# Performance work log

Hardware: AMD Instinct MI355X
Metric: run time of the kernel (lower is better)

Reference implementation:

```python
import jax, jax.numpy as jnp
import numpy as np

# Model hyperparameters (match init_kwargs)
D, N, M_DIM, L, BATCH = 10, 500, 5, 6, 1024
W_STD, B_STD, A_STD = 0.1, 0.0, 1.0


def softplus10(x):
    return jax.nn.softplus(10.0 * x) / 10.0


def setup_inputs() -> dict:
    key = jax.random.key(0)
    ks = jax.random.split(key, 7)
    w_scale = W_STD / np.sqrt(M_DIM).astype(np.float32)
    return {
        "X": jax.random.normal(ks[0], (BATCH, D), dtype=jnp.float32),
        "w_first": W_STD * jax.random.normal(ks[1], (D, N, 1, M_DIM), dtype=jnp.float32),
        "w_mid": w_scale * jax.random.normal(ks[2], (L - 2, D, N, M_DIM, M_DIM), dtype=jnp.float32),
        "w_last": w_scale * jax.random.normal(ks[3], (D, N, M_DIM, 1), dtype=jnp.float32),
        "bs": B_STD * jax.random.normal(ks[4], (L - 1, D, N, M_DIM), dtype=jnp.float32),
        "b_last": B_STD * jax.random.normal(ks[5], (D, N, 1), dtype=jnp.float32),
        "a_all": A_STD * jax.random.normal(ks[6], (L - 1, D, N, M_DIM), dtype=jnp.float32),
    }


def reference(X, w_first, w_mid, w_last, bs, b_last, a_all):
    # X: [M, d] -> phis: [M, d, n, 1]
    Mb = X.shape[0]
    phis = jnp.broadcast_to(X[:, :, None, None], (Mb, D, N, 1))
    phidots = jnp.ones_like(phis)  # [M, d, n, 1]

    ws = [w_first] + [w_mid[i] for i in range(L - 2)]
    for l in range(L - 1):
        W = softplus10(ws[l])                                    # [d,n,k,m]
        pre = jnp.einsum('mjik,jikl->mjil', phis, W) + bs[l]     # [M,d,n,m]
        ta = jnp.tanh(a_all[l])                                  # [d,n,m]
        tanhdot = 1.0 - jnp.tanh(pre) ** 2                       # tanh'(pre)
        phidots = jnp.einsum('mjik,jikl->mjil', phidots, W) * (1.0 + ta * tanhdot)
        phis = pre + jnp.tanh(pre) * ta

    Wl = softplus10(w_last)                                      # [d,n,m,1]
    pre = jnp.einsum('mjik,jikl->mjil', phis, Wl) + b_last       # [M,d,n,1]
    s = jax.nn.sigmoid(pre)
    phidots = jnp.einsum('mjik,jikl->mjil', phidots, Wl) * (s * (1.0 - s))

    fm = jax.lax.stop_gradient(-jnp.log(phidots + 1e-10))        # [M,d,n,1]
    fm = jnp.min(jnp.mean(fm, axis=1, keepdims=True), axis=2, keepdims=True)
    return jnp.squeeze(phidots, -1), fm.reshape(-1)              # ([M,d,n], [M])
```

## Files before the change

### kernel.cpp

```cpp
#include <hip/hip_runtime.h>
#include <math.h>

#define D_ 10
#define N_ 500
#define REC 164

typedef float f32x2 __attribute__((ext_vector_type(2)));

__device__ __forceinline__ float fexp2(float x){ float r; asm("v_exp_f32 %0, %1" : "=v"(r) : "v"(x)); return r; }
__device__ __forceinline__ float flog2(float x){ float r; asm("v_log_f32 %0, %1" : "=v"(r) : "v"(x)); return r; }
__device__ __forceinline__ float frcp (float x){ float r; asm("v_rcp_f32 %0, %1" : "=v"(r) : "v"(x)); return r; }

#define LOG2E 1.4426950408889634f
#define LN2   0.6931471805599453f

__device__ __forceinline__ float fast_tanh(float x){
  float e = fexp2(x * (2.0f*LOG2E));
  return 1.0f - 2.0f*frcp(e + 1.0f);
}
__device__ __forceinline__ float softplus10(float x){
  float e = fexp2(x * (10.0f*LOG2E));
  return (0.1f*LN2) * flog2(1.0f + e);
}

__device__ __forceinline__ f32x2 pk_fma_blo(f32x2 a, f32x2 w, f32x2 c){
  f32x2 d; asm("v_pk_fma_f32 %0, %1, %2, %3 op_sel:[0,0,0] op_sel_hi:[1,0,1]"
               : "=v"(d) : "v"(a), "s"(w), "v"(c)); return d; }
__device__ __forceinline__ f32x2 pk_fma_bhi(f32x2 a, f32x2 w, f32x2 c){
  f32x2 d; asm("v_pk_fma_f32 %0, %1, %2, %3 op_sel:[0,1,0] op_sel_hi:[1,1,1]"
               : "=v"(d) : "v"(a), "s"(w), "v"(c)); return d; }
__device__ __forceinline__ f32x2 pk_mul_blo(f32x2 a, f32x2 w){
  f32x2 d; asm("v_pk_mul_f32 %0, %1, %2 op_sel:[0,0] op_sel_hi:[1,0]"
               : "=v"(d) : "v"(a), "s"(w)); return d; }
__device__ __forceinline__ f32x2 pk_mul_bhi(f32x2 a, f32x2 w){
  f32x2 d; asm("v_pk_mul_f32 %0, %1, %2 op_sel:[0,1] op_sel_hi:[1,1]"
               : "=v"(d) : "v"(a), "s"(w)); return d; }
__device__ __forceinline__ f32x2 pk_mul(f32x2 a, f32x2 b){
  f32x2 d; asm("v_pk_mul_f32 %0, %1, %2" : "=v"(d) : "v"(a), "v"(b)); return d; }
__device__ __forceinline__ f32x2 pk_add(f32x2 a, f32x2 b){
  f32x2 d; asm("v_pk_add_f32 %0, %1, %2" : "=v"(d) : "v"(a), "v"(b)); return d; }
__device__ __forceinline__ f32x2 pk_nfma(f32x2 a, f32x2 b, f32x2 c){
  f32x2 d; asm("v_pk_fma_f32 %0, %1, %2, %3 neg_lo:[1,0,0] neg_hi:[1,0,0]"
               : "=v"(d) : "v"(a), "v"(b), "v"(c)); return d; }

#define LD2(off)        (*(const f32x2*)(r + ((off) & ~1)))
#define FMA_B(a, off, c) (((off)&1) ? pk_fma_bhi((a), LD2(off), (c)) : pk_fma_blo((a), LD2(off), (c)))
#define MUL_B(a, off)    (((off)&1) ? pk_mul_bhi((a), LD2(off))      : pk_mul_blo((a), LD2(off)))

__global__ __launch_bounds__(256) void tennet_prep(
    const float* __restrict__ w_first, const float* __restrict__ w_mid,
    const float* __restrict__ w_last, const float* __restrict__ bs,
    const float* __restrict__ b_last, const float* __restrict__ a_all,
    float* __restrict__ rec)
{
  int rid = blockIdx.x*4 + (threadIdx.x >> 6);
  int lane = threadIdx.x & 63;
  int d = rid / N_;
  int n = rid - d*N_;
  float* dst = rec + rid*REC;
  for (int i = lane; i < 161; i += 64) {
    float v;
    if (i < 5)        v = softplus10(w_first[(d*N_+n)*5 + i]);
    else if (i < 10)  v = bs[(d*N_+n)*5 + (i-5)];
    else if (i < 15)  v = fast_tanh(a_all[(d*N_+n)*5 + (i-10)]);
    else if (i < 155) {
      int q = i - 15; int l = q/35; int r2 = q - l*35;
      if (r2 < 25) {
        int j = r2/5, k = r2 - (r2/5)*5;
        v = softplus10(w_mid[((l*D_+d)*N_+n)*25 + k*5 + j]);
      } else if (r2 < 30) {
        v = bs[(((l+1)*D_+d)*N_+n)*5 + (r2-25)];
      } else {
        v = fast_tanh(a_all[(((l+1)*D_+d)*N_+n)*5 + (r2-30)]);
      }
    }
    else if (i < 160) v = softplus10(w_last[(d*N_+n)*5 + (i-155)]);
    else              v = b_last[d*N_+n];
    dst[i] = v;
  }
}

__global__ __launch_bounds__(1024) void tennet_main(
    const float* __restrict__ X, const float* __restrict__ rec,
    float* __restrict__ out0)
{
  __shared__ float tr[128*17];
  int bid = blockIdx.x;
  int mb  = bid & 7;
  int nch = (bid >> 3) & 31;
  int d   = bid >> 8;
  int n0 = nch*16;
  int t = threadIdx.x;
  int wv = __builtin_amdgcn_readfirstlane(t >> 6);
  int lane = t & 63;
  int n = n0 + wv;
  int nr = (n < N_) ? n : (N_-1);
  const float* r = rec + (d*N_ + nr)*REC;
  int m0 = mb*128 + lane;

  f32x2 x;
  x.x = X[m0*D_ + d];
  x.y = X[(m0+64)*D_ + d];

  const f32x2 ONE = {1.0f, 1.0f};
  const f32x2 TWO = {2.0f, 2.0f};
  const f32x2 K2  = {2.0f*LOG2E, 2.0f*LOG2E};
  const f32x2 NL2E = {-LOG2E, -LOG2E};

  f32x2 phis[5], phid[5];
  #pragma unroll
  for (int j = 0; j < 5; ++j) {
    f32x2 pre = FMA_B(x, j, MUL_B(ONE, 5+j));
    f32x2 tt = pk_mul(pre, K2);
    f32x2 e; e.x = fexp2(tt.x); e.y = fexp2(tt.y);
    f32x2 p1 = pk_add(e, ONE);
    f32x2 rc; rc.x = frcp(p1.x); rc.y = frcp(p1.y);
    f32x2 th = pk_nfma(TWO, rc, ONE);
    f32x2 td = pk_nfma(th, th, ONE);
    f32x2 u  = FMA_B(td, 10+j, ONE);
    phid[j] = MUL_B(u, j);
    phis[j] = FMA_B(th, 10+j, pre);
  }
  #pragma unroll
  for (int l = 0; l < 4; ++l) {
    const int base = 15 + l*35;
    f32x2 nphis[5], nphid[5];
    #pragma unroll
    for (int j = 0; j < 5; ++j) {
      f32x2 pre = FMA_B(phis[0], base + j*5, MUL_B(ONE, base + 25 + j));
      f32x2 pd  = MUL_B(phid[0], base + j*5);
      #pragma unroll
      for (int k = 1; k < 5; ++k) {
        pre = FMA_B(phis[k], base + j*5 + k, pre);
        pd  = FMA_B(phid[k], base + j*5 + k, pd);
      }
      f32x2 tt = pk_mul(pre, K2);
      f32x2 e; e.x = fexp2(tt.x); e.y = fexp2(tt.y);
      f32x2 p1 = pk_add(e, ONE);
      f32x2 rc; rc.x = frcp(p1.x); rc.y = frcp(p1.y);
      f32x2 th = pk_nfma(TWO, rc, ONE);
      f32x2 td = pk_nfma(th, th, ONE);
      f32x2 u  = FMA_B(td, base + 30 + j, ONE);
      nphid[j] = pk_mul(pd, u);
      nphis[j] = FMA_B(th, base + 30 + j, pre);
    }
    #pragma unroll
    for (int j = 0; j < 5; ++j){ phis[j]=nphis[j]; phid[j]=nphid[j]; }
  }
  f32x2 pre = FMA_B(phis[0], 155, MUL_B(ONE, 160));
  f32x2 pd  = MUL_B(phid[0], 155);
  #pragma unroll
  for (int k = 1; k < 5; ++k) {
    pre = FMA_B(phis[k], 155 + k, pre);
    pd  = FMA_B(phid[k], 155 + k, pd);
  }
  f32x2 tt = pk_mul(pre, NL2E);
  f32x2 e; e.x = fexp2(tt.x); e.y = fexp2(tt.y);
  f32x2 p1 = pk_add(e, ONE);
  f32x2 sg; sg.x = frcp(p1.x); sg.y = frcp(p1.y);
  f32x2 om = pk_nfma(sg, ONE, ONE);
  f32x2 res = pk_mul(pk_mul(pd, sg), om);

  tr[lane*17 + wv] = res.x;
  tr[(lane+64)*17 + wv] = res.y;
  __syncthreads();
  int tn = t & 15;
  #pragma unroll
  for (int rr = (t >> 4); rr < 128; rr += 64) {
    if (n0 + tn < N_)
      out0[((mb*128 + rr)*D_ + d)*N_ + n0 + tn] = tr[rr*17 + tn];
  }
}

__global__ __launch_bounds__(512) void tennet_fm(
    const float* __restrict__ out0, float* __restrict__ fm)
{
  int m = blockIdx.x;
  int t = threadIdx.x;
  float val = INFINITY;
  if (t < N_) {
    float acc = 0.0f;
    #pragma unroll
    for (int d = 0; d < D_; ++d) {
      float v = out0[(m*D_ + d)*N_ + t];
      acc += flog2(v + 1e-10f);
    }
    val = -acc * (LN2 / (float)D_);
  }
  #pragma unroll
  for (int off = 32; off; off >>= 1) {
    float o = __shfl_down(val, off, 64);
    val = fminf(val, o);
  }
  __shared__ float red[8];
  int wid = t >> 6;
  if ((t & 63) == 0) red[wid] = val;
  __syncthreads();
  if (t == 0) {
    float v = red[0];
    #pragma unroll
    for (int ww = 1; ww < 8; ++ww) v = fminf(v, red[ww]);
    fm[m] = v;
  }
}

extern "C" void kernel_launch(void* const* d_in, const int* in_sizes, int n_in,
                              void* d_out, int out_size, void* d_ws, size_t ws_size,
                              hipStream_t stream) {
  const float* X       = (const float*)d_in[0];
  const float* w_first = (const float*)d_in[1];
  const float* w_mid   = (const float*)d_in[2];
  const float* w_last  = (const float*)d_in[3];
  const float* bs      = (const float*)d_in[4];
  const float* b_last  = (const float*)d_in[5];
  const float* a_all   = (const float*)d_in[6];
  float* out0 = (float*)d_out;
  float* fm   = out0 + 1024*D_*N_;
  float* rec  = (float*)d_ws;

  tennet_prep<<<(D_*N_)/4, 256, 0, stream>>>(w_first, w_mid, w_last, bs, b_last, a_all, rec);
  tennet_main<<<10*32*8, 1024, 0, stream>>>(X, rec, out0);
  tennet_fm<<<1024, 512, 0, stream>>>(out0, fm);
}
```

Baseline: 66.47 us.

## Share one reciprocal across paired lanes and shrink main kernel blocks to 8 waves

The tanh and sigmoid activations now compute a single reciprocal of the product of the two packed denominators and recover each reciprocal with a multiply, halving the transcendental v_rcp count. The main kernel moves from 16 waves per block over 16 n-values to 8 waves over 8 n-values, with a matching grid and transpose buffer. This cuts padding waste (500 n-values now fill 504 slots instead of 512) and gives the scheduler finer blocks. The shared reciprocal risks overflow or underflow when both exp terms are large.

```diff
diff --git a/kernel.cpp b/kernel.cpp
--- a/kernel.cpp
+++ b/kernel.cpp
@@ -46,6 +46,19 @@
 #define LD2(off)        (*(const f32x2*)(r + ((off) & ~1)))
 #define FMA_B(a, off, c) (((off)&1) ? pk_fma_bhi((a), LD2(off), (c)) : pk_fma_blo((a), LD2(off), (c)))
 #define MUL_B(a, off)    (((off)&1) ? pk_mul_bhi((a), LD2(off))      : pk_mul_blo((a), LD2(off)))
+
+__device__ __forceinline__ void act_tanh(f32x2 pre, f32x2 ONE, f32x2 TWO, f32x2 K2,
+                                         f32x2* th, f32x2* td){
+  f32x2 tt = pk_mul(pre, K2);
+  f32x2 e; e.x = fexp2(tt.x); e.y = fexp2(tt.y);
+  f32x2 p1 = pk_add(e, ONE);
+  float pr = p1.x * p1.y;
+  float rr = frcp(pr);
+  f32x2 rc; rc.x = p1.y * rr; rc.y = p1.x * rr;
+  f32x2 t = pk_nfma(TWO, rc, ONE);
+  *th = t;
+  *td = pk_nfma(t, t, ONE);
+}
 
 __global__ __launch_bounds__(256) void tennet_prep(
     const float* __restrict__ w_first, const float* __restrict__ w_mid,
@@ -80,16 +93,17 @@
   }
 }
 
-__global__ __launch_bounds__(1024) void tennet_main(
+__global__ __launch_bounds__(512) void tennet_main(
     const float* __restrict__ X, const float* __restrict__ rec,
     float* __restrict__ out0)
 {
-  __shared__ float tr[128*17];
+  __shared__ float tr[128*9];
   int bid = blockIdx.x;
   int mb  = bid & 7;
-  int nch = (bid >> 3) & 31;
-  int d   = bid >> 8;
-  int n0 = nch*16;
+  int q   = bid >> 3;
+  int d   = q / 63;
+  int nch = q - d*63;
+  int n0 = nch*8;
   int t = threadIdx.x;
   int wv = __builtin_amdgcn_readfirstlane(t >> 6);
   int lane = t & 63;
@@ -111,14 +125,10 @@
   #pragma unroll
   for (int j = 0; j < 5; ++j) {
     f32x2 pre = FMA_B(x, j, MUL_B(ONE, 5+j));
-    f32x2 tt = pk_mul(pre, K2);
-    f32x2 e; e.x = fexp2(tt.x); e.y = fexp2(tt.y);
-    f32x2 p1 = pk_add(e, ONE);
-    f32x2 rc; rc.x = frcp(p1.x); rc.y = frcp(p1.y);
-    f32x2 th = pk_nfma(TWO, rc, ONE);
-    f32x2 td = pk_nfma(th, th, ONE);
-    f32x2 u  = FMA_B(td, 10+j, ONE);
-    phid[j] = MUL_B(u, j);
+    f32x2 th, td;
+    act_tanh(pre, ONE, TWO, K2, &th, &td);
+    f32x2 uf = FMA_B(td, 10+j, ONE);
+    phid[j] = MUL_B(uf, j);
     phis[j] = FMA_B(th, 10+j, pre);
   }
   #pragma unroll
@@ -134,14 +144,10 @@
         pre = FMA_B(phis[k], base + j*5 + k, pre);
         pd  = FMA_B(phid[k], base + j*5 + k, pd);
       }
-      f32x2 tt = pk_mul(pre, K2);
-      f32x2 e; e.x = fexp2(tt.x); e.y = fexp2(tt.y);
-      f32x2 p1 = pk_add(e, ONE);
-      f32x2 rc; rc.x = frcp(p1.x); rc.y = frcp(p1.y);
-      f32x2 th = pk_nfma(TWO, rc, ONE);
-      f32x2 td = pk_nfma(th, th, ONE);
-      f32x2 u  = FMA_B(td, base + 30 + j, ONE);
-      nphid[j] = pk_mul(pd, u);
+      f32x2 th, td;
+      act_tanh(pre, ONE, TWO, K2, &th, &td);
+      f32x2 uf = FMA_B(td, base + 30 + j, ONE);
+      nphid[j] = pk_mul(pd, uf);
       nphis[j] = FMA_B(th, base + 30 + j, pre);
     }
     #pragma unroll
@@ -157,18 +163,21 @@
   f32x2 tt = pk_mul(pre, NL2E);
   f32x2 e; e.x = fexp2(tt.x); e.y = fexp2(tt.y);
   f32x2 p1 = pk_add(e, ONE);
-  f32x2 sg; sg.x = frcp(p1.x); sg.y = frcp(p1.y);
+  float prd = p1.x * p1.y;
+  float rrc = frcp(prd);
+  f32x2 sg; sg.x = p1.y * rrc; sg.y = p1.x * rrc;
   f32x2 om = pk_nfma(sg, ONE, ONE);
   f32x2 res = pk_mul(pk_mul(pd, sg), om);
 
-  tr[lane*17 + wv] = res.x;
-  tr[(lane+64)*17 + wv] = res.y;
+  tr[lane*9 + wv]      = res.x;
+  tr[(lane+64)*9 + wv] = res.y;
   __syncthreads();
-  int tn = t & 15;
-  #pragma unroll
-  for (int rr = (t >> 4); rr < 128; rr += 64) {
+  int tn = t & 7;
+  #pragma unroll
+  for (int p = 0; p < 2; ++p) {
+    int rr2 = (t >> 3) + p*64;
     if (n0 + tn < N_)
-      out0[((mb*128 + rr)*D_ + d)*N_ + n0 + tn] = tr[rr*17 + tn];
+      out0[((mb*128 + rr2)*D_ + d)*N_ + n0 + tn] = tr[rr2*9 + tn];
   }
 }
 
@@ -219,6 +228,6 @@
   float* rec  = (float*)d_ws;
 
   tennet_prep<<<(D_*N_)/4, 256, 0, stream>>>(w_first, w_mid, w_last, bs, b_last, a_all, rec);
-  tennet_main<<<10*32*8, 1024, 0, stream>>>(X, rec, out0);
+  tennet_main<<<10*63*8, 512, 0, stream>>>(X, rec, out0);
   tennet_fm<<<1024, 512, 0, stream>>>(out0, fm);
 }
```

Result: no change. 67.44 us (+1.5%).
